# Optimization experiments

Measured on AMD Instinct MI355X. Metric: run time of the kernel, lower is better.

The kernel has to match this reference:

```python
import jax, jax.numpy as jnp
import numpy as np
from jax import lax

B, H, W, C = 8, 64, 64, 256
OUT = 1024          # channels (final conv filters)
KS = 3              # kernel_size
GROUP_DIV = 1
N_GROUPS = C // GROUP_DIV  # 256 -> depthwise-style grouped convs
DN = ('NHWC', 'HWIO', 'NHWC')
EPS = 1e-5


def setup_inputs() -> dict:
    key = jax.random.key(0)
    ks = jax.random.split(key, 6)
    x = jax.random.normal(ks[0], (B, H, W, C), jnp.float32)
    w_spatial = jax.random.normal(ks[1], (B, KS, KS, C // N_GROUPS, C), jnp.float32) * 0.05
    w_pointwise = jax.random.normal(ks[2], (B, 1, 1, C // N_GROUPS, C), jnp.float32) * 0.05
    bias = jax.random.normal(ks[3], (B, C), jnp.float32) * 0.05
    conv_w = jax.random.normal(ks[4], (KS, KS, C, OUT), jnp.float32) * (1.0 / np.sqrt(KS * KS * C))
    conv_b = jnp.zeros((OUT,), jnp.float32)
    return {"x": x, "w_spatial": w_spatial, "w_pointwise": w_pointwise,
            "bias": bias, "conv_w": conv_w, "conv_b": conv_b}


def _instance_norm(x):
    # TF: (x - mean) / (std + eps), population std over H,W per sample/channel
    mean = jnp.mean(x, axis=(1, 2), keepdims=True)
    std = jnp.sqrt(jnp.mean((x - mean) ** 2, axis=(1, 2), keepdims=True))
    return (x - mean) / (std + EPS)


def _per_sample(xi, ws, wp, b):
    # xi: [H,W,C]; ws: [ks,ks,1,C]; wp: [1,1,1,C]; b: [C]
    y = lax.conv_general_dilated(xi[None], ws, (1, 1), 'SAME',
                                 dimension_numbers=DN,
                                 feature_group_count=N_GROUPS)
    y = lax.conv_general_dilated(y, wp, (1, 1), 'VALID',
                                 dimension_numbers=DN,
                                 feature_group_count=N_GROUPS) + b
    return y[0]


def reference(x, w_spatial, w_pointwise, bias, conv_w, conv_b):
    x = _instance_norm(x)
    # batched per-sample dynamic grouped spatial + pointwise conv
    x = jax.vmap(_per_sample)(x, w_spatial, w_pointwise, bias)  # [B,H,W,C]
    # shared 3x3 SAME conv C -> OUT with bias
    y = lax.conv_general_dilated(x, conv_w, (1, 1), 'SAME',
                                 dimension_numbers=DN) + conv_b
    return y
```

## Files before the change

### kernel.cpp

```cpp
#include <hip/hip_runtime.h>
#include <hip/hip_bf16.h>
#include <cstdint>
#include <cstddef>

constexpr int Bn   = 8;
constexpr int Hn   = 64;
constexpr int Wn   = 64;
constexpr int Cn   = 256;
constexpr int OUTC = 1024;
constexpr int HPAD = 66;
constexpr int WPAD = 66;
#define EPS 1e-5f

typedef __attribute__((ext_vector_type(4))) float f32x4;
typedef __bf16 bf16x8 __attribute__((ext_vector_type(8)));

__device__ __forceinline__ void gload_lds16(const void* g, void* l) {
    __builtin_amdgcn_global_load_lds(
        (__attribute__((address_space(1))) void*)g,
        (__attribute__((address_space(3))) void*)l,
        16, 0, 0);
}

__global__ __launch_bounds__(256) void k0_transpose_w(const float* __restrict__ conv_w,
                                                      __hip_bfloat16* __restrict__ wT) {
    __shared__ float tile[64][65];
    const int tap = blockIdx.x;
    const int ct  = blockIdx.y;
    const int ot  = blockIdx.z;
    const int t   = threadIdx.x;
    const int lo  = t & 63;
    const int cq  = t >> 6;

#pragma unroll
    for (int k = 0; k < 16; ++k) {
        int ci = k * 4 + cq;
        tile[lo][ci] = conv_w[((size_t)(tap * Cn + ct * 64 + ci)) * OUTC + ot * 64 + lo];
    }
    __syncthreads();
#pragma unroll
    for (int k = 0; k < 16; ++k) {
        int oo = k * 4 + cq;
        wT[((size_t)(tap * OUTC + ot * 64 + oo)) * Cn + ct * 64 + lo] =
            __float2bfloat16(tile[oo][lo]);
    }
}

__global__ __launch_bounds__(1024) void k1_stats_partial(const float* __restrict__ x,
                                                         float* __restrict__ ps,
                                                         float* __restrict__ pq) {
    __shared__ float sb[2][4][256];
    const int bh = blockIdx.x;
    const int tid = threadIdx.x;
    const int c = tid & 255;
    const int s = tid >> 8;
    const float* row = x + (size_t)bh * Wn * Cn + (size_t)s * 16 * Cn + c;
    float sm = 0.f, q = 0.f;
#pragma unroll
    for (int w = 0; w < 16; ++w) {
        float v = row[(size_t)w * Cn];
        sm += v; q += v * v;
    }
    sb[0][s][c] = sm; sb[1][s][c] = q;
    __syncthreads();
    if (s == 0) {
        float S = 0.f, Q = 0.f;
#pragma unroll
        for (int k = 0; k < 4; ++k) { S += sb[0][k][c]; Q += sb[1][k][c]; }
        ps[bh * Cn + c] = S;
        pq[bh * Cn + c] = Q;
    }
}

__global__ __launch_bounds__(1024) void k2_stats_final(const float* __restrict__ ps,
                                                       const float* __restrict__ pq,
                                                       float* __restrict__ scale,
                                                       float* __restrict__ shift) {
    __shared__ float sb[2][4][256];
    const int b = blockIdx.x;
    const int tid = threadIdx.x;
    const int c = tid & 255;
    const int qd = tid >> 8;
    float S = 0.f, Q = 0.f;
#pragma unroll 4
    for (int i = 0; i < 16; ++i) {
        int h = qd * 16 + i;
        S += ps[(b * Hn + h) * Cn + c];
        Q += pq[(b * Hn + h) * Cn + c];
    }
    sb[0][qd][c] = S; sb[1][qd][c] = Q;
    __syncthreads();
    if (qd == 0) {
        float s2 = 0.f, q2 = 0.f;
#pragma unroll
        for (int k = 0; k < 4; ++k) { s2 += sb[0][k][c]; q2 += sb[1][k][c]; }
        const float inv = 1.f / (float)(Hn * Wn);
        float mean = s2 * inv;
        float var  = fmaxf(q2 * inv - mean * mean, 0.f);
        float sc   = 1.f / (sqrtf(var) + EPS);
        scale[b * Cn + c] = sc;
        shift[b * Cn + c] = -mean * sc;
    }
}

__global__ __launch_bounds__(256) void k3_dwconv(const float* __restrict__ x,
                                                 const float* __restrict__ w_sp,
                                                 const float* __restrict__ w_pw,
                                                 const float* __restrict__ bias,
                                                 const float* __restrict__ scale,
                                                 const float* __restrict__ shift,
                                                 __hip_bfloat16* __restrict__ tpad) {
    const int bq = blockIdx.x;
    const int wq = bq & 3;
    const int bh = bq >> 2;
    const int b  = bh / HPAD;
    const int hp = bh - b * HPAD;
    const int c  = threadIdx.x;
    __hip_bfloat16* orow = tpad + ((size_t)(b * HPAD + hp)) * WPAD * Cn + c;
    const __hip_bfloat16 z = __float2bfloat16(0.f);

    if (hp == 0 || hp == HPAD - 1) {
        int wlo = wq * 17, whi = wlo + 17 < WPAD ? wlo + 17 : WPAD;
        for (int wp = wlo; wp < whi; ++wp) orow[(size_t)wp * Cn] = z;
        return;
    }
    const int h = hp - 1;
    const float sc = scale[b * Cn + c];
    const float sh = shift[b * Cn + c];
    float w9[9];
#pragma unroll
    for (int k = 0; k < 9; ++k) w9[k] = w_sp[(b * 9 + k) * Cn + c];
    const float pw = w_pw[b * Cn + c];
    const float bv = bias[b * Cn + c];
    const float* xb = x + (size_t)b * Hn * Wn * Cn + c;

    bool rv[3];
#pragma unroll
    for (int r = 0; r < 3; ++r) { int rr = h - 1 + r; rv[r] = (rr >= 0 && rr < Hn); }

    if (wq == 0) orow[0] = z;
    if (wq == 3) orow[(size_t)(WPAD - 1) * Cn] = z;

    const int w0 = wq * 16;
    float win[3][3];
#pragma unroll
    for (int r = 0; r < 3; ++r) {
        win[r][0] = (rv[r] && w0 > 0)
                    ? (xb[((size_t)(h - 1 + r) * Wn + (w0 - 1)) * Cn] * sc + sh) : 0.f;
        win[r][1] = rv[r] ? (xb[((size_t)(h - 1 + r) * Wn + w0) * Cn] * sc + sh) : 0.f;
    }
    for (int i = 0; i < 16; ++i) {
        const int w = w0 + i;
#pragma unroll
        for (int r = 0; r < 3; ++r)
            win[r][2] = (rv[r] && (w + 1) < Wn)
                        ? (xb[((size_t)(h - 1 + r) * Wn + (w + 1)) * Cn] * sc + sh) : 0.f;
        float y = 0.f;
#pragma unroll
        for (int r = 0; r < 3; ++r)
#pragma unroll
            for (int qq = 0; qq < 3; ++qq)
                y += win[r][qq] * w9[r * 3 + qq];
        orow[(size_t)(w + 1) * Cn] = __float2bfloat16(y * pw + bv);
#pragma unroll
        for (int r = 0; r < 3; ++r) { win[r][0] = win[r][1]; win[r][1] = win[r][2]; }
    }
}

constexpr int KSTEPS = 72;
constexpr int BUFSZ  = 32768;

__global__ __launch_bounds__(512, 2) void k4_gemm(const __hip_bfloat16* __restrict__ tpad,
                                                  const __hip_bfloat16* __restrict__ wT,
                                                  const float* __restrict__ conv_b,
                                                  float* __restrict__ out) {
    __shared__ __align__(16) char smem[4 * BUFSZ];

    const int tid  = threadIdx.x;
    const int lane = tid & 63;
    const int wv   = tid >> 6;
    const int wm   = wv >> 2;
    const int wn   = wv & 3;
    const int g    = lane >> 4, l15 = lane & 15;

    const int bid = blockIdx.x;
    const int mt  = (bid & 7) * 16 + ((bid >> 3) & 15);
    const int nt  = bid >> 7;
    const int pixbase = mt * 256;
    const int b       = mt >> 4;
    const int hbase   = (mt & 15) * 4;
    const int obase   = nt * 256;

    int aoff[2], boff[2];
#pragma unroll
    for (int j = 0; j < 2; ++j) {
        int u = j * 512 + tid;
        int r = u >> 3, p = u & 7;
        int l = p ^ (r & 7);
        int pix = 2 * r + (l >> 2);
        int hh  = hbase + (pix >> 6);
        int ww  = pix & 63;
        aoff[j] = ((b * HPAD + hh) * WPAD + ww) * Cn + (l & 3) * 8;
        boff[j] = (obase + 2 * r + (l >> 2)) * Cn + (l & 3) * 8;
    }

    auto stageHalf = [&](int s, int half) {
        const int tap = s >> 3, ks = s & 7;
        const int kh  = tap / 3, kw = tap - 3 * kh;
        char* buf = smem + (s & 3) * BUFSZ;
        if (half == 0) {
            const __hip_bfloat16* aS = tpad + ((kh * WPAD + kw) * Cn + ks * 32);
            gload_lds16(aS + aoff[0], buf + (size_t)(0 * 512 + wv * 64) * 16);
            gload_lds16(aS + aoff[1], buf + (size_t)(1 * 512 + wv * 64) * 16);
        } else {
            const __hip_bfloat16* bS = wT + (size_t)tap * (OUTC * Cn) + ks * 32;
            gload_lds16(bS + boff[0], buf + 16384 + (size_t)(0 * 512 + wv * 64) * 16);
            gload_lds16(bS + boff[1], buf + 16384 + (size_t)(1 * 512 + wv * 64) * 16);
        }
    };

    const int slot = ((((l15 & 1) << 2) | g) ^ ((l15 >> 1) & 7)) * 16;
    const int aRd  = wm * 8192 + (l15 >> 1) * 128 + slot;
    const int bRd  = 16384 + wn * 4096 + (l15 >> 1) * 128 + slot;

    f32x4 acc[8][4] = {};

    stageHalf(0, 0); stageHalf(0, 1);
    stageHalf(1, 0); stageHalf(1, 1);
    asm volatile("s_waitcnt vmcnt(4)" ::: "memory");
    __builtin_amdgcn_s_barrier();
    __builtin_amdgcn_sched_barrier(0);

#pragma unroll 1
    for (int t = 0; t < KSTEPS; ++t) {
        char* cb = smem + (t & 3) * BUFSZ;
        const bool st = (t + 2 < KSTEPS);
        bf16x8 bfr[4], aP[4], aQ[4];

        if (st) stageHalf(t + 2, 0);
#pragma unroll
        for (int n = 0; n < 4; ++n)
            bfr[n] = *(const bf16x8*)(cb + bRd + n * 1024);
#pragma unroll
        for (int m = 0; m < 4; ++m)
            aP[m] = *(const bf16x8*)(cb + aRd + m * 1024);
        __builtin_amdgcn_sched_barrier(0);
        __builtin_amdgcn_s_barrier();
        asm volatile("s_waitcnt lgkmcnt(0)" ::: "memory");
        __builtin_amdgcn_sched_barrier(0);
        __builtin_amdgcn_s_setprio(1);
#pragma unroll
        for (int m = 0; m < 4; ++m)
#pragma unroll
            for (int n = 0; n < 4; ++n)
                acc[m][n] = __builtin_amdgcn_mfma_f32_16x16x32_bf16(
                    aP[m], bfr[n], acc[m][n], 0, 0, 0);
        __builtin_amdgcn_s_setprio(0);
        __builtin_amdgcn_sched_barrier(0);
        __builtin_amdgcn_s_barrier();

        if (st) stageHalf(t + 2, 1);
#pragma unroll
        for (int m = 0; m < 4; ++m)
            aQ[m] = *(const bf16x8*)(cb + aRd + (m + 4) * 1024);
        __builtin_amdgcn_sched_barrier(0);
        __builtin_amdgcn_s_barrier();
        asm volatile("s_waitcnt lgkmcnt(0)" ::: "memory");
        __builtin_amdgcn_sched_barrier(0);
        __builtin_amdgcn_s_setprio(1);
#pragma unroll
        for (int m = 0; m < 4; ++m)
#pragma unroll
            for (int n = 0; n < 4; ++n)
                acc[m + 4][n] = __builtin_amdgcn_mfma_f32_16x16x32_bf16(
                    aQ[m], bfr[n], acc[m + 4][n], 0, 0, 0);
        __builtin_amdgcn_s_setprio(0);
        __builtin_amdgcn_sched_barrier(0);

        if (t + 1 < KSTEPS) {
            if (st) { asm volatile("s_waitcnt vmcnt(4)" ::: "memory"); }
            else    { asm volatile("s_waitcnt vmcnt(0)" ::: "memory"); }
            __builtin_amdgcn_s_barrier();
            __builtin_amdgcn_sched_barrier(0);
        }
    }

    float cb2[4];
#pragma unroll
    for (int n = 0; n < 4; ++n) cb2[n] = conv_b[obase + wn * 64 + n * 16 + l15];
#pragma unroll
    for (int m = 0; m < 8; ++m) {
#pragma unroll
        for (int j = 0; j < 4; ++j) {
            int r = pixbase + wm * 128 + m * 16 + g * 4 + j;
            float* orow = out + (size_t)r * OUTC + obase + wn * 64 + l15;
#pragma unroll
            for (int n = 0; n < 4; ++n)
                orow[n * 16] = acc[m][n][j] + cb2[n];
        }
    }
}

extern "C" void kernel_launch(void* const* d_in, const int* in_sizes, int n_in,
                              void* d_out, int out_size, void* d_ws, size_t ws_size,
                              hipStream_t stream) {
    const float* x      = (const float*)d_in[0];
    const float* w_sp   = (const float*)d_in[1];
    const float* w_pw   = (const float*)d_in[2];
    const float* bias   = (const float*)d_in[3];
    const float* conv_w = (const float*)d_in[4];
    const float* conv_b = (const float*)d_in[5];
    float* out = (float*)d_out;

    char* ws = (char*)d_ws;
    __hip_bfloat16* wT    = (__hip_bfloat16*)(ws);
    float*          ps    = (float*)(ws + 4718592);
    float*          pq    = (float*)(ws + 4718592 + 524288);
    float*          scale = (float*)(ws + 5767168);
    float*          shift = (float*)(ws + 5775360);
    __hip_bfloat16* tpad  = (__hip_bfloat16*)(ws + 5783552);

    k0_transpose_w<<<dim3(9, 4, 16), 256, 0, stream>>>(conv_w, wT);
    k1_stats_partial<<<Bn * Hn, 1024, 0, stream>>>(x, ps, pq);
    k2_stats_final<<<Bn, 1024, 0, stream>>>(ps, pq, scale, shift);
    k3_dwconv<<<Bn * HPAD * 4, 256, 0, stream>>>(x, w_sp, w_pw, bias, scale, shift, tpad);
    k4_gemm<<<512, 512, 0, stream>>>(tpad, wT, conv_b, out);
}
```

Baseline: 188.8 us.

## Restructure GEMM pipeline to 64-wide K tiles with double buffering and staggered staging

The implicit-GEMM conv kernel now stages 64-wide K slices per iteration (36 outer steps instead of 72) into two 64KB LDS buffers instead of four 32KB ones. Each outer step runs four MFMA phases. A-tile loads for the next step and B-tile loads two steps ahead are interleaved between the phases. The aim is fewer loop iterations, fewer barriers per unit of work and better load/compute overlap. The cost is more complex vmcnt accounting and the same 128KB of LDS, so occupancy is unchanged.

```diff
diff --git a/kernel.cpp b/kernel.cpp
--- a/kernel.cpp
+++ b/kernel.cpp
@@ -167,14 +167,14 @@
     }
 }
 
-constexpr int KSTEPS = 72;
-constexpr int BUFSZ  = 32768;
+constexpr int NT    = 36;
+constexpr int BUFSZ = 65536;
 
 __global__ __launch_bounds__(512, 2) void k4_gemm(const __hip_bfloat16* __restrict__ tpad,
                                                   const __hip_bfloat16* __restrict__ wT,
                                                   const float* __restrict__ conv_b,
                                                   float* __restrict__ out) {
-    __shared__ __align__(16) char smem[4 * BUFSZ];
+    __shared__ __align__(16) char smem[2 * BUFSZ];
 
     const int tid  = threadIdx.x;
     const int lane = tid & 63;
@@ -191,59 +191,47 @@
     const int hbase   = (mt & 15) * 4;
     const int obase   = nt * 256;
 
-    int aoff[2], boff[2];
-#pragma unroll
-    for (int j = 0; j < 2; ++j) {
-        int u = j * 512 + tid;
-        int r = u >> 3, p = u & 7;
-        int l = p ^ (r & 7);
-        int pix = 2 * r + (l >> 2);
+    const int lg  = (tid & 7) ^ ((tid >> 3) & 7);
+    const int rel = 2 * (tid >> 3) + (lg >> 2);
+    const int kb  = (lg & 3) * 8;
+    int aoffh[2], boffh[2];
+#pragma unroll
+    for (int h = 0; h < 2; ++h) {
+        int pix = h * 128 + rel;
         int hh  = hbase + (pix >> 6);
         int ww  = pix & 63;
-        aoff[j] = ((b * HPAD + hh) * WPAD + ww) * Cn + (l & 3) * 8;
-        boff[j] = (obase + 2 * r + (l >> 2)) * Cn + (l & 3) * 8;
-    }
-
-    auto stageHalf = [&](int s, int half) {
-        const int tap = s >> 3, ks = s & 7;
+        aoffh[h] = ((b * HPAD + hh) * WPAD + ww) * Cn + kb;
+        boffh[h] = (obase + h * 128 + rel) * Cn + kb;
+    }
+
+    auto stage = [&](int s, int isB, int h) {
+        const int tap = s >> 2, q = s & 3;
         const int kh  = tap / 3, kw = tap - 3 * kh;
-        char* buf = smem + (s & 3) * BUFSZ;
-        if (half == 0) {
-            const __hip_bfloat16* aS = tpad + ((kh * WPAD + kw) * Cn + ks * 32);
-            gload_lds16(aS + aoff[0], buf + (size_t)(0 * 512 + wv * 64) * 16);
-            gload_lds16(aS + aoff[1], buf + (size_t)(1 * 512 + wv * 64) * 16);
-        } else {
-            const __hip_bfloat16* bS = wT + (size_t)tap * (OUTC * Cn) + ks * 32;
-            gload_lds16(bS + boff[0], buf + 16384 + (size_t)(0 * 512 + wv * 64) * 16);
-            gload_lds16(bS + boff[1], buf + 16384 + (size_t)(1 * 512 + wv * 64) * 16);
+        char* dst = smem + (s & 1) * BUFSZ + isB * 32768 + h * 8192
+                  + (size_t)(wv * 64) * 16;
+        const __hip_bfloat16* src =
+            isB ? (wT + (size_t)tap * (OUTC * Cn) + q * 64 + boffh[h])
+                : (tpad + ((kh * WPAD + kw) * Cn) + q * 64 + aoffh[h]);
+        gload_lds16(src,      dst);
+        gload_lds16(src + 32, dst + 16384);
+    };
+
+    const int slot16 = ((((l15 & 1) << 2) | g) ^ ((l15 >> 1) & 7)) * 16;
+    const int aR = (wm * 64 + (l15 >> 1)) * 128 + slot16;
+    const int bR = 32768 + (wn * 32 + (l15 >> 1)) * 128 + slot16;
+
+    f32x4 acc[8][4] = {};
+    bf16x8 bfr[4], af[4];
+
+    auto phase = [&](char* cb, int mbase, int kk, bool readB, int endw) {
+        if (readB) {
+#pragma unroll
+            for (int n = 0; n < 4; ++n)
+                bfr[n] = *(const bf16x8*)(cb + bR + kk * 16384 + n * 1024);
         }
-    };
-
-    const int slot = ((((l15 & 1) << 2) | g) ^ ((l15 >> 1) & 7)) * 16;
-    const int aRd  = wm * 8192 + (l15 >> 1) * 128 + slot;
-    const int bRd  = 16384 + wn * 4096 + (l15 >> 1) * 128 + slot;
-
-    f32x4 acc[8][4] = {};
-
-    stageHalf(0, 0); stageHalf(0, 1);
-    stageHalf(1, 0); stageHalf(1, 1);
-    asm volatile("s_waitcnt vmcnt(4)" ::: "memory");
-    __builtin_amdgcn_s_barrier();
-    __builtin_amdgcn_sched_barrier(0);
-
-#pragma unroll 1
-    for (int t = 0; t < KSTEPS; ++t) {
-        char* cb = smem + (t & 3) * BUFSZ;
-        const bool st = (t + 2 < KSTEPS);
-        bf16x8 bfr[4], aP[4], aQ[4];
-
-        if (st) stageHalf(t + 2, 0);
-#pragma unroll
-        for (int n = 0; n < 4; ++n)
-            bfr[n] = *(const bf16x8*)(cb + bRd + n * 1024);
 #pragma unroll
         for (int m = 0; m < 4; ++m)
-            aP[m] = *(const bf16x8*)(cb + aRd + m * 1024);
+            af[m] = *(const bf16x8*)(cb + aR + kk * 16384 + (mbase + m) * 1024);
         __builtin_amdgcn_sched_barrier(0);
         __builtin_amdgcn_s_barrier();
         asm volatile("s_waitcnt lgkmcnt(0)" ::: "memory");
@@ -253,36 +241,35 @@
         for (int m = 0; m < 4; ++m)
 #pragma unroll
             for (int n = 0; n < 4; ++n)
-                acc[m][n] = __builtin_amdgcn_mfma_f32_16x16x32_bf16(
-                    aP[m], bfr[n], acc[m][n], 0, 0, 0);
+                acc[mbase + m][n] = __builtin_amdgcn_mfma_f32_16x16x32_bf16(
+                    af[m], bfr[n], acc[mbase + m][n], 0, 0, 0);
         __builtin_amdgcn_s_setprio(0);
         __builtin_amdgcn_sched_barrier(0);
+        if (endw == 4)      { asm volatile("s_waitcnt vmcnt(4)" ::: "memory"); }
+        else if (endw == 0) { asm volatile("s_waitcnt vmcnt(0)" ::: "memory"); }
         __builtin_amdgcn_s_barrier();
-
-        if (st) stageHalf(t + 2, 1);
-#pragma unroll
-        for (int m = 0; m < 4; ++m)
-            aQ[m] = *(const bf16x8*)(cb + aRd + (m + 4) * 1024);
         __builtin_amdgcn_sched_barrier(0);
-        __builtin_amdgcn_s_barrier();
-        asm volatile("s_waitcnt lgkmcnt(0)" ::: "memory");
-        __builtin_amdgcn_sched_barrier(0);
-        __builtin_amdgcn_s_setprio(1);
-#pragma unroll
-        for (int m = 0; m < 4; ++m)
-#pragma unroll
-            for (int n = 0; n < 4; ++n)
-                acc[m + 4][n] = __builtin_amdgcn_mfma_f32_16x16x32_bf16(
-                    aQ[m], bfr[n], acc[m + 4][n], 0, 0, 0);
-        __builtin_amdgcn_s_setprio(0);
-        __builtin_amdgcn_sched_barrier(0);
-
-        if (t + 1 < KSTEPS) {
-            if (st) { asm volatile("s_waitcnt vmcnt(4)" ::: "memory"); }
-            else    { asm volatile("s_waitcnt vmcnt(0)" ::: "memory"); }
-            __builtin_amdgcn_s_barrier();
-            __builtin_amdgcn_sched_barrier(0);
-        }
+    };
+
+    stage(0, 0, 0); stage(0, 0, 1); stage(0, 1, 0); stage(0, 1, 1);
+    stage(1, 1, 0); stage(1, 1, 1);
+    asm volatile("s_waitcnt vmcnt(4)" ::: "memory");
+    __builtin_amdgcn_s_barrier();
+    __builtin_amdgcn_sched_barrier(0);
+
+#pragma unroll 1
+    for (int T = 0; T < NT; ++T) {
+        char* cb = smem + (T & 1) * BUFSZ;
+        const bool s1 = (T + 1 < NT);
+        const bool s2 = (T + 2 < NT);
+
+        if (s1) stage(T + 1, 0, 0);
+        phase(cb, 0, 0, true,  -1);
+        if (s1) stage(T + 1, 0, 1);
+        phase(cb, 4, 0, false, -1);
+        phase(cb, 0, 1, true,  -1);
+        if (s2) { stage(T + 2, 1, 0); stage(T + 2, 1, 1); }
+        phase(cb, 4, 1, false, s2 ? 4 : 0);
     }
 
     float cb2[4];
```

Measured after the change: 184.3 us. 2.4% less time.
